# Kernel tuning notes

Hardware: AMD Instinct MI355X
Metric: run time of the kernel (lower is better)

The kernel has to match this reference:

```python
import jax, jax.numpy as jnp
import numpy as np

B, S, D, H = 8, 1024, 768, 12
E = D // H  # head_size = 64
EPS = 1e-5


def _ln(x, g, b):
    mu = jnp.mean(x, axis=-1, keepdims=True)
    var = jnp.mean(jnp.square(x - mu), axis=-1, keepdims=True)
    return (x - mu) * jax.lax.rsqrt(var + EPS) * g + b


def setup_inputs() -> dict:
    key = jax.random.key(0)
    ks = jax.random.split(key, 16)
    w = lambda k, shape: jax.random.normal(k, shape, dtype=jnp.float32) * 0.02
    return {
        "x": jax.random.normal(ks[0], (B, S, D), dtype=jnp.float32),
        "ln1_g": jnp.ones((D,), jnp.float32),
        "ln1_b": jnp.zeros((D,), jnp.float32),
        "Wq": w(ks[1], (H, D, E)),
        "bq": w(ks[2], (H, E)),
        "Wv": w(ks[3], (H, D, E)),
        "bv": w(ks[4], (H, E)),
        "Wo": w(ks[5], (H * E, D)),
        "bo": w(ks[6], (D,)),
        "ln2_g": jnp.ones((D,), jnp.float32),
        "ln2_b": jnp.zeros((D,), jnp.float32),
        "W1": w(ks[7], (D, 4 * D)),
        "b1": w(ks[8], (4 * D,)),
        "W2": w(ks[9], (4 * D, D)),
        "b2": w(ks[10], (D,)),
    }


def reference(x, ln1_g, ln1_b, Wq, bq, Wv, bv, Wo, bo, ln2_g, ln2_b, W1, b1, W2, b2):
    d_k = x.shape[-1]
    h = _ln(x, ln1_g, ln1_b)
    # Faithful quirk: keys use the QUERY projection (k = self.query(x) in source).
    q = jnp.einsum('bsd,hde->bhse', h, Wq) + bq[None, :, None, :]
    k = q  # same projection, same input -> identical tensor
    v = jnp.einsum('bsd,hde->bhse', h, Wv) + bv[None, :, None, :]
    # Faithful quirk: scale uses full d_k, not head_size.
    scores = jnp.einsum('bhse,bhte->bhst', q, k) * (d_k ** -0.5)
    prob = jax.nn.softmax(scores, axis=-1)
    o = jnp.einsum('bhst,bhte->bhse', prob, v)  # [B,H,S,E]
    o = o.transpose(0, 2, 1, 3).reshape(x.shape[0], x.shape[1], -1)  # concat heads
    x = x + o @ Wo + bo
    h2 = _ln(x, ln2_g, ln2_b)
    mlp = jax.nn.gelu(h2 @ W1 + b1, approximate=False) @ W2 + b2
    return x + mlp
```

## Files before the change

### kernel.cpp

```cpp
#include <hip/hip_runtime.h>
#include <stdint.h>


typedef __attribute__((ext_vector_type(8))) short s8v;
typedef __attribute__((ext_vector_type(4))) float f32x4;
typedef __attribute__((ext_vector_type(4))) unsigned short us4v;

__device__ __forceinline__ unsigned short f2b(float f) {
  union { float f; unsigned u; } v; v.f = f;
  unsigned r = v.u + 0x7FFFu + ((v.u >> 16) & 1u);
  return (unsigned short)(r >> 16);
}

__device__ __forceinline__ void g2l16(const unsigned short* g, unsigned short* l) {
  __builtin_amdgcn_global_load_lds(
      (const __attribute__((address_space(1))) unsigned int*)g,
      (__attribute__((address_space(3))) unsigned int*)l, 16, 0, 0);
}

#define QSCALE 0.22816534f

__global__ __launch_bounds__(256) void repack_kernel(
    const float* __restrict__ Wq, const float* __restrict__ bq,
    const float* __restrict__ Wv, const float* __restrict__ bv,
    const float* __restrict__ Wo, const float* __restrict__ W1,
    const float* __restrict__ W2,
    unsigned short* __restrict__ Wqv_t, float* __restrict__ bias_qv,
    unsigned short* __restrict__ Wo_t, unsigned short* __restrict__ W1_t,
    unsigned short* __restrict__ W2_t)
{
  int i = blockIdx.x * 256 + threadIdx.x;
  if (i < 1536 * 768) {
    int n = i / 768, d = i % 768;
    float val;
    if (n < 768) { int h = n >> 6, e = n & 63; val = Wq[(h * 768 + d) * 64 + e] * QSCALE; }
    else { int c = n - 768; int h = c >> 6, e = c & 63; val = Wv[(h * 768 + d) * 64 + e]; }
    Wqv_t[i] = f2b(val);
  }
  if (i < 1536) bias_qv[i] = (i < 768) ? bq[i] * QSCALE : bv[i - 768];
  if (i < 768 * 768)  { int n = i / 768,  k = i % 768;  Wo_t[i] = f2b(Wo[k * 768  + n]); }
  if (i < 3072 * 768) { int n = i / 768,  k = i % 768;  W1_t[i] = f2b(W1[k * 3072 + n]); }
  if (i < 768 * 3072) { int n = i / 3072, k = i % 3072; W2_t[i] = f2b(W2[k * 768  + n]); }
}

__global__ __launch_bounds__(256) void ln_kernel(
    const float* __restrict__ x, const float* __restrict__ g,
    const float* __restrict__ b, unsigned short* __restrict__ out)
{
  __shared__ float red[4], red2[4];
  int row = blockIdx.x, t = threadIdx.x;
  const float* xr = x + (size_t)row * 768;
  float v0 = xr[t], v1 = xr[t + 256], v2 = xr[t + 512];
  float s = v0 + v1 + v2;
  #pragma unroll
  for (int m = 32; m; m >>= 1) s += __shfl_xor(s, m);
  if ((t & 63) == 0) red[t >> 6] = s;
  __syncthreads();
  float mean = (red[0] + red[1] + red[2] + red[3]) * (1.f / 768.f);
  float d0 = v0 - mean, d1 = v1 - mean, d2 = v2 - mean;
  float vs = d0 * d0 + d1 * d1 + d2 * d2;
  #pragma unroll
  for (int m = 32; m; m >>= 1) vs += __shfl_xor(vs, m);
  if ((t & 63) == 0) red2[t >> 6] = vs;
  __syncthreads();
  float var = (red2[0] + red2[1] + red2[2] + red2[3]) * (1.f / 768.f);
  float rs = rsqrtf(var + 1e-5f);
  unsigned short* o = out + (size_t)row * 768;
  o[t]       = f2b(d0 * rs * g[t]       + b[t]);
  o[t + 256] = f2b(d1 * rs * g[t + 256] + b[t + 256]);
  o[t + 512] = f2b(d2 * rs * g[t + 512] + b[t + 512]);
}

template<int NTN, int BAND>
__device__ __forceinline__ void band_map(int bid, int grid, int& m_t, int& n_t) {
  int q8 = grid >> 3;
  int mb = q8 / NTN;
  int xcd = bid & 7, idx = bid >> 3;
  int pb = BAND * NTN;
  int band = idx / pb, r = idx % pb;
  m_t = xcd * mb + band * BAND + (r % BAND);
  n_t = r / BAND;
}

template<int EPI, int N, int K>
__global__ __launch_bounds__(512, 4) void gemm128(
    const unsigned short* __restrict__ A, const unsigned short* __restrict__ Bt,
    const float* __restrict__ bias,
    const float* resid, float* out_f32,
    unsigned short* __restrict__ out_bf,
    unsigned short* __restrict__ q_out, unsigned short* __restrict__ vt_out)
{
  __shared__ __align__(16) unsigned short As_[2][8192];
  __shared__ __align__(16) unsigned short Bs_[2][8192];
  constexpr int NTN = N >> 7;
  constexpr int NT = K >> 6;
  int m_t, n_t;
  band_map<NTN, 4>(blockIdx.x, gridDim.x, m_t, n_t);
  int m0 = m_t << 7, n0 = n_t << 7;
  int t = threadIdx.x, lane = t & 63, w = t >> 6;
  int l15 = lane & 15, lg = lane >> 4;
  int wm = (w >> 2) << 6;
  int wn = (w & 3) << 5;
  int lrow = lane >> 3;
  int lxor = ((lane & 7) ^ lrow) << 3;
  const unsigned short* Abase = A + (size_t)m0 * K;
  const unsigned short* Bbase = Bt + (size_t)n0 * K;

  auto stage = [&](int buf, int tile) {
    int k0 = tile << 6;
    #pragma unroll
    for (int j = 0; j < 2; ++j) {
      int row = j * 64 + w * 8 + lrow;
      int doff = (j * 512 + w * 64) * 8;
      g2l16(&Abase[(size_t)row * K + k0 + lxor], &As_[buf][doff]);
      g2l16(&Bbase[(size_t)row * K + k0 + lxor], &Bs_[buf][doff]);
    }
  };

  f32x4 acc[4][2] = {};
  stage(0, 0);
  asm volatile("s_waitcnt vmcnt(0)" ::: "memory");
  __builtin_amdgcn_sched_barrier(0);
  __builtin_amdgcn_s_barrier();

  int cswz = (l15 & 7) << 3;
  for (int tt = 0; tt < NT; ++tt) {
    int cur = tt & 1;
    if (tt + 1 < NT) {
      stage(cur ^ 1, tt + 1);
      asm volatile("s_waitcnt vmcnt(4)" ::: "memory");
    } else {
      asm volatile("s_waitcnt vmcnt(0)" ::: "memory");
    }
    __builtin_amdgcn_sched_barrier(0);
    __builtin_amdgcn_s_barrier();
    __builtin_amdgcn_sched_barrier(0);
    const unsigned short* Ac = &As_[cur][0];
    const unsigned short* Bc = &Bs_[cur][0];
    #pragma unroll
    for (int kk = 0; kk < 2; ++kk) {
      s8v a[4], b[2];
      int col = (kk * 32 + lg * 8) ^ cswz;
      #pragma unroll
      for (int i = 0; i < 4; ++i)
        a[i] = *(const s8v*)&Ac[(wm + i * 16 + l15) * 64 + col];
      #pragma unroll
      for (int i = 0; i < 2; ++i)
        b[i] = *(const s8v*)&Bc[(wn + i * 16 + l15) * 64 + col];
      __builtin_amdgcn_s_setprio(1);
      #pragma unroll
      for (int mi = 0; mi < 4; ++mi)
        #pragma unroll
        for (int ni = 0; ni < 2; ++ni)
          acc[mi][ni] = __builtin_amdgcn_mfma_f32_16x16x32_bf16(a[mi], b[ni], acc[mi][ni], 0, 0, 0);
      __builtin_amdgcn_s_setprio(0);
    }
    if (tt + 1 < NT) {
      __builtin_amdgcn_sched_barrier(0);
      __builtin_amdgcn_s_barrier();
      __builtin_amdgcn_sched_barrier(0);
    }
  }
  #pragma unroll
  for (int mi = 0; mi < 4; ++mi) {
    #pragma unroll
    for (int ni = 0; ni < 2; ++ni) {
      int col = n0 + wn + ni * 16 + l15;
      float bs = bias[col];
      #pragma unroll
      for (int r = 0; r < 4; ++r) {
        int row = m0 + wm + mi * 16 + lg * 4 + r;
        float v = acc[mi][ni][r] + bs;
        if (EPI == 1) {
          out_f32[(size_t)row * N + col] = resid[(size_t)row * N + col] + v;
        } else if (EPI == 2) {
          float v2 = v * v;
          float z = v * fmaf(-0.10294202f, v2, -2.302026f);
          float e; asm("v_exp_f32 %0, %1" : "=v"(e) : "v"(z));
          float rcp; asm("v_rcp_f32 %0, %1" : "=v"(rcp) : "v"(e + 1.0f));
          out_bf[(size_t)row * N + col] = f2b(v * rcp);
        } else {
          if (col < 768) {
            q_out[(size_t)row * 768 + col] = f2b(v);
          } else {
            int c = col - 768; int hh = c >> 6, e = c & 63;
            int bb = row >> 10, s = row & 1023;
            vt_out[(((size_t)(bb * 12 + hh)) * 64 + e) * 1024 + s] = f2b(v);
          }
        }
      }
    }
  }
}

template<int N, int K>
__global__ __launch_bounds__(512, 6) void gemm_n64(
    const unsigned short* __restrict__ A, const unsigned short* __restrict__ Bt,
    const float* __restrict__ bias, const float* resid, float* out_f32)
{
  __shared__ __align__(16) unsigned short As_[2][8192];
  __shared__ __align__(16) unsigned short Bs_[2][4096];
  constexpr int NTN = N >> 6;
  constexpr int NT = K >> 6;
  int m_t, n_t;
  band_map<NTN, 4>(blockIdx.x, gridDim.x, m_t, n_t);
  int m0 = m_t << 7, n0 = n_t << 6;
  int t = threadIdx.x, lane = t & 63, w = t >> 6;
  int l15 = lane & 15, lg = lane >> 4;
  int wm = (w >> 1) << 5;
  int wn = (w & 1) << 5;
  int lrow = lane >> 3;
  int lxor = ((lane & 7) ^ lrow) << 3;
  const unsigned short* Abase = A + (size_t)m0 * K;
  const unsigned short* Bbase = Bt + (size_t)n0 * K;

  auto stage = [&](int buf, int tile) {
    int k0 = tile << 6;
    #pragma unroll
    for (int j = 0; j < 2; ++j) {
      int row = j * 64 + w * 8 + lrow;
      g2l16(&Abase[(size_t)row * K + k0 + lxor], &As_[buf][(j * 512 + w * 64) * 8]);
    }
    int brow = w * 8 + lrow;
    g2l16(&Bbase[(size_t)brow * K + k0 + lxor], &Bs_[buf][w * 512]);
  };

  f32x4 acc[2][2] = {};
  stage(0, 0);
  asm volatile("s_waitcnt vmcnt(0)" ::: "memory");
  __builtin_amdgcn_sched_barrier(0);
  __builtin_amdgcn_s_barrier();

  int cswz = (l15 & 7) << 3;
  for (int tt = 0; tt < NT; ++tt) {
    int cur = tt & 1;
    if (tt + 1 < NT) {
      stage(cur ^ 1, tt + 1);
      asm volatile("s_waitcnt vmcnt(3)" ::: "memory");
    } else {
      asm volatile("s_waitcnt vmcnt(0)" ::: "memory");
    }
    __builtin_amdgcn_sched_barrier(0);
    __builtin_amdgcn_s_barrier();
    __builtin_amdgcn_sched_barrier(0);
    const unsigned short* Ac = &As_[cur][0];
    const unsigned short* Bc = &Bs_[cur][0];
    #pragma unroll
    for (int kk = 0; kk < 2; ++kk) {
      s8v a[2], b[2];
      int col = (kk * 32 + lg * 8) ^ cswz;
      #pragma unroll
      for (int i = 0; i < 2; ++i)
        a[i] = *(const s8v*)&Ac[(wm + i * 16 + l15) * 64 + col];
      #pragma unroll
      for (int i = 0; i < 2; ++i)
        b[i] = *(const s8v*)&Bc[(wn + i * 16 + l15) * 64 + col];
      __builtin_amdgcn_s_setprio(1);
      #pragma unroll
      for (int mi = 0; mi < 2; ++mi)
        #pragma unroll
        for (int ni = 0; ni < 2; ++ni)
          acc[mi][ni] = __builtin_amdgcn_mfma_f32_16x16x32_bf16(a[mi], b[ni], acc[mi][ni], 0, 0, 0);
      __builtin_amdgcn_s_setprio(0);
    }
    if (tt + 1 < NT) {
      __builtin_amdgcn_sched_barrier(0);
      __builtin_amdgcn_s_barrier();
      __builtin_amdgcn_sched_barrier(0);
    }
  }
  #pragma unroll
  for (int mi = 0; mi < 2; ++mi) {
    #pragma unroll
    for (int ni = 0; ni < 2; ++ni) {
      int col = n0 + wn + ni * 16 + l15;
      float bs = bias[col];
      #pragma unroll
      for (int r = 0; r < 4; ++r) {
        int row = m0 + wm + mi * 16 + lg * 4 + r;
        float v = acc[mi][ni][r] + bs;
        out_f32[(size_t)row * N + col] = resid[(size_t)row * N + col] + v;
      }
    }
  }
}

__global__ __launch_bounds__(256, 3) void attn_kernel(
    const unsigned short* __restrict__ qk,
    const unsigned short* __restrict__ vt,
    unsigned short* __restrict__ o)
{
  __shared__ __align__(16) unsigned short Ps[4][32 * 64];
  int bid = blockIdx.x;
  int xcd = bid & 7, idx = bid >> 3;
  int bh = xcd * 12 + (idx >> 3), qt = idx & 7;
  int b = bh / 12, h = bh % 12;
  int t = threadIdx.x, lane = t & 63, w = t >> 6;
  int l15 = lane & 15, lg = lane >> 4;
  int wq0 = w << 5;
  size_t qrow0 = (size_t)b * 1024 + qt * 128;
  size_t krow0 = (size_t)b * 1024;
  size_t vbase = ((size_t)bh) * 64 * 1024;
  int cswz = (l15 & 7) << 3;
  unsigned short* myPs = &Ps[w][0];

  s8v qf[2][2];
  #pragma unroll
  for (int ni = 0; ni < 2; ++ni)
    #pragma unroll
    for (int kk = 0; kk < 2; ++kk)
      qf[ni][kk] = *(const s8v*)&qk[(qrow0 + wq0 + ni * 16 + l15) * 768 +
                                    h * 64 + kk * 32 + lg * 8];

  f32x4 oacc[4][2] = {};
  float lsum[2] = {0.f, 0.f};

  for (int kt = 0; kt < 16; ++kt) {
    s8v a[4][2];
    #pragma unroll
    for (int i = 0; i < 4; ++i)
      #pragma unroll
      for (int kk = 0; kk < 2; ++kk)
        a[i][kk] = *(const s8v*)&qk[(krow0 + kt * 64 + i * 16 + l15) * 768 +
                                    h * 64 + kk * 32 + lg * 8];
    f32x4 st[4][2] = {};
    #pragma unroll
    for (int kk = 0; kk < 2; ++kk)
      #pragma unroll
      for (int mi = 0; mi < 4; ++mi)
        #pragma unroll
        for (int ni = 0; ni < 2; ++ni)
          st[mi][ni] = __builtin_amdgcn_mfma_f32_16x16x32_bf16(a[mi][kk], qf[ni][kk], st[mi][ni], 0, 0, 0);
    #pragma unroll
    for (int ni = 0; ni < 2; ++ni) {
      int prow = (ni * 16 + l15) * 64;
      #pragma unroll
      for (int mi = 0; mi < 4; ++mi) {
        float p0, p1, p2, p3;
        asm("v_exp_f32 %0, %1" : "=v"(p0) : "v"(st[mi][ni][0]));
        asm("v_exp_f32 %0, %1" : "=v"(p1) : "v"(st[mi][ni][1]));
        asm("v_exp_f32 %0, %1" : "=v"(p2) : "v"(st[mi][ni][2]));
        asm("v_exp_f32 %0, %1" : "=v"(p3) : "v"(st[mi][ni][3]));
        lsum[ni] += (p0 + p1) + (p2 + p3);
        unsigned lo, hi;
        asm("v_cvt_pk_bf16_f32 %0, %1, %2" : "=v"(lo) : "v"(p0), "v"(p1));
        asm("v_cvt_pk_bf16_f32 %0, %1, %2" : "=v"(hi) : "v"(p2), "v"(p3));
        unsigned long long pk = (unsigned long long)lo | ((unsigned long long)hi << 32);
        *(unsigned long long*)&myPs[prow + ((mi * 16 + lg * 4) ^ cswz)] = pk;
      }
    }
    #pragma unroll
    for (int kk = 0; kk < 2; ++kk) {
      int col = (kk * 32 + lg * 8) ^ cswz;
      s8v vv[4], bp[2];
      #pragma unroll
      for (int i = 0; i < 4; ++i)
        vv[i] = *(const s8v*)&vt[vbase + (size_t)(i * 16 + l15) * 1024 +
                                 kt * 64 + kk * 32 + lg * 8];
      #pragma unroll
      for (int i = 0; i < 2; ++i)
        bp[i] = *(const s8v*)&myPs[(i * 16 + l15) * 64 + col];
      #pragma unroll
      for (int ei = 0; ei < 4; ++ei)
        #pragma unroll
        for (int ni = 0; ni < 2; ++ni)
          oacc[ei][ni] = __builtin_amdgcn_mfma_f32_16x16x32_bf16(vv[ei], bp[ni], oacc[ei][ni], 0, 0, 0);
    }
  }
  #pragma unroll
  for (int ni = 0; ni < 2; ++ni) {
    float s = lsum[ni];
    s += __shfl_xor(s, 16);
    s += __shfl_xor(s, 32);
    float inv = 1.f / s;
    int q = wq0 + ni * 16 + l15;
    size_t obase = (qrow0 + q) * 768 + h * 64;
    #pragma unroll
    for (int ei = 0; ei < 4; ++ei) {
      us4v ov;
      #pragma unroll
      for (int r = 0; r < 4; ++r) ov[r] = f2b(oacc[ei][ni][r] * inv);
      *(us4v*)&o[obase + ei * 16 + lg * 4] = ov;
    }
  }
}

extern "C" void kernel_launch(void* const* d_in, const int* in_sizes, int n_in,
                              void* d_out, int out_size, void* d_ws, size_t ws_size,
                              hipStream_t stream)
{
  const float* x     = (const float*)d_in[0];
  const float* ln1_g = (const float*)d_in[1];
  const float* ln1_b = (const float*)d_in[2];
  const float* Wq    = (const float*)d_in[3];
  const float* bq    = (const float*)d_in[4];
  const float* Wv    = (const float*)d_in[5];
  const float* bv    = (const float*)d_in[6];
  const float* Wo    = (const float*)d_in[7];
  const float* bo    = (const float*)d_in[8];
  const float* ln2_g = (const float*)d_in[9];
  const float* ln2_b = (const float*)d_in[10];
  const float* W1    = (const float*)d_in[11];
  const float* b1    = (const float*)d_in[12];
  const float* W2    = (const float*)d_in[13];
  const float* b2    = (const float*)d_in[14];
  float* out = (float*)d_out;

  char* ws = (char*)d_ws;
  size_t off = 0;
  auto alloc = [&](size_t bytes) -> void* {
    void* p = ws + off; off += (bytes + 255) & ~(size_t)255; return p;
  };
  unsigned short* Wqv_t  = (unsigned short*)alloc(1536ull * 768 * 2);
  float*          bias_qv= (float*)         alloc(1536ull * 4);
  unsigned short* Wo_t   = (unsigned short*)alloc(768ull * 768 * 2);
  unsigned short* W1_t   = (unsigned short*)alloc(3072ull * 768 * 2);
  unsigned short* W2_t   = (unsigned short*)alloc(768ull * 3072 * 2);
  unsigned short* h_bf   = (unsigned short*)alloc(8192ull * 768 * 2);
  unsigned short* q_bf   = (unsigned short*)alloc(8192ull * 768 * 2);
  unsigned short* v_t    = (unsigned short*)alloc(96ull * 64 * 1024 * 2);
  unsigned short* o_bf   = (unsigned short*)alloc(8192ull * 768 * 2);
  unsigned short* h2_bf  = (unsigned short*)alloc(8192ull * 768 * 2);
  unsigned short* m1_bf  = (unsigned short*)alloc(8192ull * 3072 * 2);

  repack_kernel<<<9216, 256, 0, stream>>>(Wq, bq, Wv, bv, Wo, W1, W2,
                                          Wqv_t, bias_qv, Wo_t, W1_t, W2_t);
  ln_kernel<<<8192, 256, 0, stream>>>(x, ln1_g, ln1_b, h_bf);
  gemm128<3, 1536, 768><<<768, 512, 0, stream>>>(h_bf, Wqv_t, bias_qv,
      nullptr, nullptr, nullptr, q_bf, v_t);
  attn_kernel<<<768, 256, 0, stream>>>(q_bf, v_t, o_bf);
  gemm128<1, 768, 768><<<384, 512, 0, stream>>>(o_bf, Wo_t, bo,
      x, out, nullptr, nullptr, nullptr);
  ln_kernel<<<8192, 256, 0, stream>>>(out, ln2_g, ln2_b, h2_bf);
  gemm128<2, 3072, 768><<<1536, 512, 0, stream>>>(h2_bf, W1_t, b1,
      nullptr, nullptr, m1_bf, nullptr, nullptr);
  gemm_n64<768, 3072><<<768, 512, 0, stream>>>(m1_bf, W2_t, b2, out, out);
}
```

Before: 304.1 us.

## Double-buffer K and V tiles in LDS via async global-to-LDS loads

The attention kernel now stages each 64-row K tile and 64-column V tile into shared memory with global_load_lds, double-buffered, and prefetches the next tile while computing the current one. All four waves then read K and V from swizzled LDS instead of each wave loading them directly from global memory. This removes redundant per-wave global reads and hides load latency. In exchange it adds 32KB of LDS, which may reduce occupancy, plus two block barriers per iteration.

```diff
diff --git a/kernel.cpp b/kernel.cpp
--- a/kernel.cpp
+++ b/kernel.cpp
@@ -290,6 +290,8 @@
     const unsigned short* __restrict__ vt,
     unsigned short* __restrict__ o)
 {
+  __shared__ __align__(16) unsigned short Ks[2][64 * 64];
+  __shared__ __align__(16) unsigned short Vs[2][64 * 64];
   __shared__ __align__(16) unsigned short Ps[4][32 * 64];
   int bid = blockIdx.x;
   int xcd = bid & 7, idx = bid >> 3;
@@ -304,6 +306,21 @@
   int cswz = (l15 & 7) << 3;
   unsigned short* myPs = &Ps[w][0];
 
+  int srow = t >> 3;
+  int scsw = ((t & 7) << 3) ^ ((srow & 7) << 3);
+  const unsigned short* ksrc = &qk[(krow0 + srow) * 768 + h * 64 + scsw];
+  const unsigned short* vsrc = &vt[vbase + (size_t)srow * 1024 + scsw];
+
+  auto stage = [&](int buf, int kt) {
+    const unsigned short* kp = ksrc + (size_t)kt * 64 * 768;
+    const unsigned short* vp = vsrc + kt * 64;
+    #pragma unroll
+    for (int j = 0; j < 2; ++j) {
+      g2l16(kp + (size_t)j * 32 * 768, &Ks[buf][(j * 256 + w * 64) * 8]);
+      g2l16(vp + (size_t)j * 32 * 1024, &Vs[buf][(j * 256 + w * 64) * 8]);
+    }
+  };
+
   s8v qf[2][2];
   #pragma unroll
   for (int ni = 0; ni < 2; ++ni)
@@ -315,22 +332,37 @@
   f32x4 oacc[4][2] = {};
   float lsum[2] = {0.f, 0.f};
 
+  stage(0, 0);
+  asm volatile("s_waitcnt vmcnt(0)" ::: "memory");
+  __builtin_amdgcn_sched_barrier(0);
+  __builtin_amdgcn_s_barrier();
+
   for (int kt = 0; kt < 16; ++kt) {
-    s8v a[4][2];
-    #pragma unroll
-    for (int i = 0; i < 4; ++i)
-      #pragma unroll
-      for (int kk = 0; kk < 2; ++kk)
-        a[i][kk] = *(const s8v*)&qk[(krow0 + kt * 64 + i * 16 + l15) * 768 +
-                                    h * 64 + kk * 32 + lg * 8];
+    int buf = kt & 1;
+    if (kt + 1 < 16) {
+      stage(buf ^ 1, kt + 1);
+      asm volatile("s_waitcnt vmcnt(4)" ::: "memory");
+    } else {
+      asm volatile("s_waitcnt vmcnt(0)" ::: "memory");
+    }
+    __builtin_amdgcn_sched_barrier(0);
+    __builtin_amdgcn_s_barrier();
+    __builtin_amdgcn_sched_barrier(0);
+    const unsigned short* Kb = Ks[buf];
+    const unsigned short* Vb = Vs[buf];
     f32x4 st[4][2] = {};
     #pragma unroll
-    for (int kk = 0; kk < 2; ++kk)
+    for (int kk = 0; kk < 2; ++kk) {
+      int col = (kk * 32 + lg * 8) ^ cswz;
+      s8v a[4];
+      #pragma unroll
+      for (int i = 0; i < 4; ++i) a[i] = *(const s8v*)&Kb[(i * 16 + l15) * 64 + col];
       #pragma unroll
       for (int mi = 0; mi < 4; ++mi)
         #pragma unroll
         for (int ni = 0; ni < 2; ++ni)
-          st[mi][ni] = __builtin_amdgcn_mfma_f32_16x16x32_bf16(a[mi][kk], qf[ni][kk], st[mi][ni], 0, 0, 0);
+          st[mi][ni] = __builtin_amdgcn_mfma_f32_16x16x32_bf16(a[mi], qf[ni][kk], st[mi][ni], 0, 0, 0);
+    }
     #pragma unroll
     for (int ni = 0; ni < 2; ++ni) {
       int prow = (ni * 16 + l15) * 64;
@@ -354,17 +386,19 @@
       int col = (kk * 32 + lg * 8) ^ cswz;
       s8v vv[4], bp[2];
       #pragma unroll
-      for (int i = 0; i < 4; ++i)
-        vv[i] = *(const s8v*)&vt[vbase + (size_t)(i * 16 + l15) * 1024 +
-                                 kt * 64 + kk * 32 + lg * 8];
-      #pragma unroll
-      for (int i = 0; i < 2; ++i)
-        bp[i] = *(const s8v*)&myPs[(i * 16 + l15) * 64 + col];
+      for (int i = 0; i < 4; ++i) vv[i] = *(const s8v*)&Vb[(i * 16 + l15) * 64 + col];
+      #pragma unroll
+      for (int i = 0; i < 2; ++i) bp[i] = *(const s8v*)&myPs[(i * 16 + l15) * 64 + col];
       #pragma unroll
       for (int ei = 0; ei < 4; ++ei)
         #pragma unroll
         for (int ni = 0; ni < 2; ++ni)
           oacc[ei][ni] = __builtin_amdgcn_mfma_f32_16x16x32_bf16(vv[ei], bp[ni], oacc[ei][ni], 0, 0, 0);
+    }
+    if (kt + 1 < 16) {
+      __builtin_amdgcn_sched_barrier(0);
+      __builtin_amdgcn_s_barrier();
+      __builtin_amdgcn_sched_barrier(0);
     }
   }
   #pragma unroll
```

After: 251.4 us. 17.3% less time.
